# Kernel tuning notes

Measured on AMD Instinct MI355X. Metric: run time of the kernel, lower is better.

The kernel has to match this reference:

```python
import jax, jax.numpy as jnp
import numpy as np
from jax import lax

BASE = 10000.0
N_STATE = 4096
N_HEAD = 32
H_DIM = N_STATE // N_HEAD          # 128
NUM_ROT = H_DIM // 2               # 64
BATCH, SEQ = 4, 2048


def setup_inputs() -> dict:
    key = jax.random.key(0)
    k1, k2, k3, k4 = jax.random.split(key, 4)
    x = jax.random.normal(k1, (BATCH, SEQ, N_STATE), dtype=jnp.float32)
    thetas = jax.random.normal(k2, (NUM_ROT,), dtype=jnp.float32) * 0.1
    rotation_pairs = jax.random.uniform(k3, (NUM_ROT, 2), dtype=jnp.float32) * H_DIM
    theta_scale = jnp.ones((1,), dtype=jnp.float32)
    rotation_matrix = jnp.eye(H_DIM, dtype=jnp.float32) + 0.02 * jax.random.normal(k4, (H_DIM, H_DIM), dtype=jnp.float32)
    inv_freq = (1.0 / BASE ** (jnp.arange(0, H_DIM, 2, dtype=jnp.float32) / H_DIM)).astype(jnp.float32)
    return {"x": x, "thetas": thetas, "rotation_pairs": rotation_pairs,
            "theta_scale": theta_scale, "rotation_matrix": rotation_matrix,
            "inv_freq": inv_freq, "n_head": N_HEAD}


def _apply(x, thetas, rotation_pairs, theta_scale, rotation_matrix, inv_freq, n_head):
    B, S, n_state = x.shape
    h_dim = rotation_matrix.shape[0]
    xf = x.reshape(B, S, n_head, h_dim).reshape(-1, h_dim)  # [B*S*H, h_dim]

    idx = rotation_pairs.astype(jnp.int32)          # [R,2] Givens pair indices
    th = thetas * theta_scale[0]                    # [R]

    def body(xc, inp):
        i, j, t = inp
        c, s = jnp.cos(t), jnp.sin(t)
        xi = xc[:, i]
        xj = xc[:, j]
        same = (i == j)
        # x @ G touches only columns i and j (matches torch G construction,
        # including the i==j overwrite case where G[i,i] ends as cos)
        vi = jnp.where(same, xi * c, xi * c + xj * s)
        vj = jnp.where(same, xi * c, -xi * s + xj * c)
        xc = xc.at[:, i].set(vi)
        xc = xc.at[:, j].set(vj)
        return xc, None

    xf, _ = lax.scan(body, xf, (idx[:, 0], idx[:, 1], th))
    xf = xf @ rotation_matrix                       # learned h_dim x h_dim mix
    xh = xf.reshape(B, S, n_head, h_dim)

    pos = jnp.arange(S, dtype=jnp.float32)
    sinusoid = pos[:, None] * inv_freq[None, :]     # [S, h_dim/2]
    sin = jnp.sin(sinusoid)[None, :, None, :]
    cos = jnp.cos(sinusoid)[None, :, None, :]
    x1 = xh[..., ::2]
    x2 = xh[..., 1::2]
    out = jnp.concatenate([x1 * cos - x2 * sin, x1 * sin + x2 * cos], axis=-1)
    return out.reshape(B, S, n_state)


def reference(x, thetas, rotation_pairs, theta_scale, rotation_matrix, inv_freq, n_head):
    return _apply(x, thetas, rotation_pairs, theta_scale, rotation_matrix, inv_freq, n_head)
```

## Files before the change

### kernel.cpp

```cpp
#include <hip/hip_runtime.h>
#include <math.h>

#define SEQ_LEN 2048
#define NROWS (4 * 2048 * 32)
#define NSTRIPS (NROWS / 16)

typedef short bf16x8 __attribute__((ext_vector_type(8)));
typedef float f32x4 __attribute__((ext_vector_type(4)));

__device__ __forceinline__ unsigned short f2bf(float f) {
    union { float f; unsigned int i; } v; v.f = f;
    unsigned int r = v.i + 0x7FFFu + ((v.i >> 16) & 1u);
    return (unsigned short)(r >> 16);
}

__global__ void prep_kernel(const float* __restrict__ thetas,
                            const float* __restrict__ pairs,
                            const float* __restrict__ tscale,
                            const float* __restrict__ rotmat,
                            unsigned short* __restrict__ Bsw) {
    __shared__ float M[128][128];
    const int t = threadIdx.x;
    for (int d = 0; d < 128; ++d) M[d][t] = rotmat[d * 128 + t];
    const float scale = tscale[0];
    for (int r = 63; r >= 0; --r) {
        int i = (int)pairs[2 * r];
        int j = (int)pairs[2 * r + 1];
        i = min(max(i, 0), 127); j = min(max(j, 0), 127);
        const float th = thetas[r] * scale;
        const float c = cosf(th), s = sinf(th);
        if (i == j) {
            M[i][t] *= c;
        } else {
            const float a = M[i][t], b = M[j][t];
            M[i][t] = c * a - s * b;
            M[j][t] = s * a + c * b;
        }
    }
    __syncthreads();
    for (int idx = t; idx < 32 * 64; idx += 128) {
        const int f = idx >> 6, lane = idx & 63;
        const int kk = f >> 3, nt = f & 7;
        const int krow = kk * 32 + (lane >> 4) * 8;
        const int col = nt * 16 + (lane & 15);
        unsigned short* dst = Bsw + (size_t)idx * 8;
#pragma unroll
        for (int j2 = 0; j2 < 8; ++j2) dst[j2] = f2bf(M[krow + j2][col]);
    }
}

__global__ __launch_bounds__(256) void rope_kernel(
        const float* __restrict__ x,
        const unsigned short* __restrict__ Bsw,
        const float* __restrict__ invfreq,
        float* __restrict__ out) {
    const int lane = threadIdx.x & 63;
    const int wave = (int)(blockIdx.x * (blockDim.x >> 6) + (threadIdx.x >> 6));
    const int nwaves = (int)(gridDim.x * (blockDim.x >> 6));
    const int m = lane & 15;
    const int quad = lane >> 4;

    bf16x8 Bf[32];
    const bf16x8* Bp = (const bf16x8*)Bsw;
#pragma unroll
    for (int f = 0; f < 32; ++f) Bf[f] = Bp[f * 64 + lane];

    const float invf = invfreq[lane];
    const int kq = m >> 1;
    const bool oddl = (m & 1);

    for (int strip = wave; strip < NSTRIPS; strip += nwaves) {
        const int r0 = strip * 16;
        const float* xrow = x + (size_t)(r0 + m) * 128 + quad * 8;
        bf16x8 A[4];
#pragma unroll
        for (int kk = 0; kk < 4; ++kk) {
            const f32x4 lo = *(const f32x4*)(xrow + kk * 32);
            const f32x4 hi = *(const f32x4*)(xrow + kk * 32 + 4);
            bf16x8 a;
#pragma unroll
            for (int e = 0; e < 4; ++e) {
                a[e]     = (short)f2bf(lo[e]);
                a[e + 4] = (short)f2bf(hi[e]);
            }
            A[kk] = a;
        }

        const int s_pos = (r0 >> 5) & (SEQ_LEN - 1);
        float sn_l, cs_l;
        sincosf((float)s_pos * invf, &sn_l, &cs_l);

        f32x4 acc[8];
#pragma unroll
        for (int nt = 0; nt < 8; ++nt) acc[nt] = (f32x4){0.f, 0.f, 0.f, 0.f};

#pragma unroll
        for (int kk = 0; kk < 4; ++kk) {
#pragma unroll
            for (int nt = 0; nt < 8; ++nt)
                acc[nt] = __builtin_amdgcn_mfma_f32_16x16x32_bf16(
                    A[kk], Bf[kk * 8 + nt], acc[nt], 0, 0, 0);
        }

        float* orow = out + (size_t)r0 * 128;
#pragma unroll
        for (int nt = 0; nt < 8; ++nt) {
            const int k = nt * 8 + kq;
            const float c = __shfl(cs_l, k, 64);
            const float sn = __shfl(sn_l, k, 64);
            const float ss = oddl ? sn : -sn;
            const int outcol = oddl ? (64 + k) : k;
#pragma unroll
            for (int rr = 0; rr < 4; ++rr) {
                const float v = acc[nt][rr];
                const float p = __shfl_xor(v, 1, 64);
                const float val = fmaf(p, ss, v * c);
                orow[(size_t)(quad * 4 + rr) * 128 + outcol] = val;
            }
        }
    }
}

extern "C" void kernel_launch(void* const* d_in, const int* in_sizes, int n_in,
                              void* d_out, int out_size, void* d_ws, size_t ws_size,
                              hipStream_t stream) {
    const float* x      = (const float*)d_in[0];
    const float* thetas = (const float*)d_in[1];
    const float* pairs  = (const float*)d_in[2];
    const float* tscale = (const float*)d_in[3];
    const float* rotmat = (const float*)d_in[4];
    const float* invfr  = (const float*)d_in[5];
    float* out = (float*)d_out;
    unsigned short* Bsw = (unsigned short*)d_ws;

    prep_kernel<<<1, 128, 0, stream>>>(thetas, pairs, tscale, rotmat, Bsw);
    rope_kernel<<<1024, 256, 0, stream>>>(x, Bsw, invfr, out);
}
```

Before: 279.9 us.

## Permute B columns, stage B in LDS, use nontemporal stores and hardware bf16 convert

The prep kernel now precomputes Givens cos/sin and indices into shared memory and permutes B's columns so even and odd outputs land in separate MFMA tiles. This removes the shuffle_xor pairing in the RoPE epilogue. The main kernel keeps B in LDS instead of 32 VGPR vectors, aiming for higher occupancy, and doubles the grid. It also uses packed bf16 conversion intrinsics and nontemporal output stores. The trade-off is an LDS read for every MFMA operand and 32KB of LDS per block.

```diff
diff --git a/kernel.cpp b/kernel.cpp
--- a/kernel.cpp
+++ b/kernel.cpp
@@ -1,4 +1,5 @@
 #include <hip/hip_runtime.h>
+#include <hip/hip_bf16.h>
 #include <math.h>
 
 #define SEQ_LEN 2048
@@ -20,15 +21,23 @@
                             const float* __restrict__ rotmat,
                             unsigned short* __restrict__ Bsw) {
     __shared__ float M[128][128];
+    __shared__ float Cv[64], Sv[64];
+    __shared__ int   Iv[64], Jv[64];
     const int t = threadIdx.x;
+    if (t < 64) {
+        const float th = thetas[t] * tscale[0];
+        Cv[t] = cosf(th);
+        Sv[t] = sinf(th);
+        int i = (int)pairs[2 * t];
+        int j = (int)pairs[2 * t + 1];
+        Iv[t] = min(max(i, 0), 127);
+        Jv[t] = min(max(j, 0), 127);
+    }
     for (int d = 0; d < 128; ++d) M[d][t] = rotmat[d * 128 + t];
-    const float scale = tscale[0];
+    __syncthreads();
     for (int r = 63; r >= 0; --r) {
-        int i = (int)pairs[2 * r];
-        int j = (int)pairs[2 * r + 1];
-        i = min(max(i, 0), 127); j = min(max(j, 0), 127);
-        const float th = thetas[r] * scale;
-        const float c = cosf(th), s = sinf(th);
+        const int i = Iv[r], j = Jv[r];
+        const float c = Cv[r], s = Sv[r];
         if (i == j) {
             M[i][t] *= c;
         } else {
@@ -42,80 +51,89 @@
         const int f = idx >> 6, lane = idx & 63;
         const int kk = f >> 3, nt = f & 7;
         const int krow = kk * 32 + (lane >> 4) * 8;
-        const int col = nt * 16 + (lane & 15);
+        const int n = nt * 16 + (lane & 15);
+        const int col = (n < 64) ? (2 * n) : (2 * (n - 64) + 1);
         unsigned short* dst = Bsw + (size_t)idx * 8;
 #pragma unroll
         for (int j2 = 0; j2 < 8; ++j2) dst[j2] = f2bf(M[krow + j2][col]);
     }
 }
 
-__global__ __launch_bounds__(256) void rope_kernel(
+__global__ __launch_bounds__(256, 4) void rope_kernel(
         const float* __restrict__ x,
         const unsigned short* __restrict__ Bsw,
         const float* __restrict__ invfreq,
         float* __restrict__ out) {
+    __shared__ f32x4 Blds[2048];
+    {
+        const f32x4* src = (const f32x4*)Bsw;
+#pragma unroll
+        for (int i = 0; i < 8; ++i)
+            Blds[threadIdx.x + 256 * i] = src[threadIdx.x + 256 * i];
+    }
+    __syncthreads();
+
     const int lane = threadIdx.x & 63;
     const int wave = (int)(blockIdx.x * (blockDim.x >> 6) + (threadIdx.x >> 6));
     const int nwaves = (int)(gridDim.x * (blockDim.x >> 6));
     const int m = lane & 15;
     const int quad = lane >> 4;
-
-    bf16x8 Bf[32];
-    const bf16x8* Bp = (const bf16x8*)Bsw;
-#pragma unroll
-    for (int f = 0; f < 32; ++f) Bf[f] = Bp[f * 64 + lane];
+    const bf16x8* Bf = (const bf16x8*)Blds;
 
     const float invf = invfreq[lane];
-    const int kq = m >> 1;
-    const bool oddl = (m & 1);
 
     for (int strip = wave; strip < NSTRIPS; strip += nwaves) {
         const int r0 = strip * 16;
         const float* xrow = x + (size_t)(r0 + m) * 128 + quad * 8;
-        bf16x8 A[4];
+        f32x4 lo[4], hi[4];
 #pragma unroll
         for (int kk = 0; kk < 4; ++kk) {
-            const f32x4 lo = *(const f32x4*)(xrow + kk * 32);
-            const f32x4 hi = *(const f32x4*)(xrow + kk * 32 + 4);
-            bf16x8 a;
-#pragma unroll
-            for (int e = 0; e < 4; ++e) {
-                a[e]     = (short)f2bf(lo[e]);
-                a[e + 4] = (short)f2bf(hi[e]);
-            }
-            A[kk] = a;
+            lo[kk] = *(const f32x4*)(xrow + kk * 32);
+            hi[kk] = *(const f32x4*)(xrow + kk * 32 + 4);
         }
 
         const int s_pos = (r0 >> 5) & (SEQ_LEN - 1);
         float sn_l, cs_l;
         sincosf((float)s_pos * invf, &sn_l, &cs_l);
 
+        bf16x8 A[4];
+#pragma unroll
+        for (int kk = 0; kk < 4; ++kk) {
+            union { __hip_bfloat162 h; unsigned int u; } c0, c1, c2, c3;
+            c0.h = __float22bfloat162_rn(make_float2(lo[kk][0], lo[kk][1]));
+            c1.h = __float22bfloat162_rn(make_float2(lo[kk][2], lo[kk][3]));
+            c2.h = __float22bfloat162_rn(make_float2(hi[kk][0], hi[kk][1]));
+            c3.h = __float22bfloat162_rn(make_float2(hi[kk][2], hi[kk][3]));
+            union { unsigned int u[4]; bf16x8 v; } a;
+            a.u[0] = c0.u; a.u[1] = c1.u; a.u[2] = c2.u; a.u[3] = c3.u;
+            A[kk] = a.v;
+        }
+
         f32x4 acc[8];
 #pragma unroll
         for (int nt = 0; nt < 8; ++nt) acc[nt] = (f32x4){0.f, 0.f, 0.f, 0.f};
 
 #pragma unroll
-        for (int kk = 0; kk < 4; ++kk) {
+        for (int kk = 0; kk < 4; ++kk)
 #pragma unroll
             for (int nt = 0; nt < 8; ++nt)
                 acc[nt] = __builtin_amdgcn_mfma_f32_16x16x32_bf16(
-                    A[kk], Bf[kk * 8 + nt], acc[nt], 0, 0, 0);
-        }
+                    A[kk], Bf[(kk * 8 + nt) * 64 + lane], acc[nt], 0, 0, 0);
 
-        float* orow = out + (size_t)r0 * 128;
+        float* orow = out + (size_t)(r0 + quad * 4) * 128;
 #pragma unroll
-        for (int nt = 0; nt < 8; ++nt) {
-            const int k = nt * 8 + kq;
+        for (int nt = 0; nt < 4; ++nt) {
+            const int k = nt * 16 + m;
             const float c = __shfl(cs_l, k, 64);
-            const float sn = __shfl(sn_l, k, 64);
-            const float ss = oddl ? sn : -sn;
-            const int outcol = oddl ? (64 + k) : k;
+            const float s = __shfl(sn_l, k, 64);
 #pragma unroll
             for (int rr = 0; rr < 4; ++rr) {
-                const float v = acc[nt][rr];
-                const float p = __shfl_xor(v, 1, 64);
-                const float val = fmaf(p, ss, v * c);
-                orow[(size_t)(quad * 4 + rr) * 128 + outcol] = val;
+                const float ye = acc[nt][rr];
+                const float yo = acc[nt + 4][rr];
+                __builtin_nontemporal_store(ye * c - yo * s,
+                                            &orow[(size_t)rr * 128 + k]);
+                __builtin_nontemporal_store(ye * s + yo * c,
+                                            &orow[(size_t)rr * 128 + 64 + k]);
             }
         }
     }
@@ -134,5 +152,5 @@
     unsigned short* Bsw = (unsigned short*)d_ws;
 
     prep_kernel<<<1, 128, 0, stream>>>(thetas, pairs, tscale, rotmat, Bsw);
-    rope_kernel<<<1024, 256, 0, stream>>>(x, Bsw, invfr, out);
+    rope_kernel<<<2048, 256, 0, stream>>>(x, Bsw, invfr, out);
 }
```

Result: slower. 308.1 us (+10.1%).
